# Performance work log

Hardware: AMD Instinct MI355X
Metric: run time of the kernel (lower is better)

Reference implementation:

```python
import jax, jax.numpy as jnp
import numpy as np

DIM, SSM, RNN = 1024, 64, 128


def setup_inputs() -> dict:
    key = jax.random.key(0)
    ks = jax.random.split(key, 16)
    s = 0.02
    B, N = 8, 2048
    return {
        'x': jax.random.normal(ks[0], (B, N, DIM), jnp.float32),
        'A': jax.random.normal(ks[1], (SSM, SSM), jnp.float32) * s,
        'Bw': jax.random.normal(ks[2], (SSM, DIM), jnp.float32) * s,
        'Bb': jnp.zeros((SSM,), jnp.float32),
        'Cw': jax.random.normal(ks[3], (DIM, SSM), jnp.float32) * s,
        'Cb': jnp.zeros((DIM,), jnp.float32),
        'Dw': jax.random.normal(ks[4], (DIM, DIM), jnp.float32) * s,
        'Db': jnp.zeros((DIM,), jnp.float32),
        'W_ih': jax.random.normal(ks[5], (3 * RNN, DIM), jnp.float32) * s,
        'b_ih': jnp.zeros((3 * RNN,), jnp.float32),
        'W_hh': jax.random.normal(ks[6], (3 * RNN, RNN), jnp.float32) * s,
        'b_hh': jnp.zeros((3 * RNN,), jnp.float32),
        'proj_w': jax.random.normal(ks[7], (DIM, RNN), jnp.float32) * s,
        'proj_b': jnp.zeros((DIM,), jnp.float32),
        'gate_w': jax.random.normal(ks[8], (2, DIM), jnp.float32) * s,
        'gate_b': jnp.zeros((2,), jnp.float32),
    }


def reference(x, A, Bw, Bb, Cw, Cb, Dw, Db, W_ih, b_ih, W_hh, b_hh, proj_w, proj_b, gate_w, gate_b):
    B, N, D = x.shape
    R = W_hh.shape[1]
    # Precompute all input-side projections once (time-parallel GEMMs).
    bx = jnp.einsum('bnd,sd->bns', x, Bw) + Bb            # [B,N,SSM]
    dx = jnp.einsum('bnd,ed->bne', x, Dw) + Db            # [B,N,D]
    gx = jax.nn.sigmoid(jnp.einsum('bnd,gd->bng', x, gate_w) + gate_b)  # [B,N,2]
    ih = jnp.einsum('bnd,rd->bnr', x, W_ih) + b_ih        # [B,N,3R]
    # time-major for scan
    bx_t = jnp.swapaxes(bx, 0, 1)
    dx_t = jnp.swapaxes(dx, 0, 1)
    gx_t = jnp.swapaxes(gx, 0, 1)
    ih_t = jnp.swapaxes(ih, 0, 1)

    h_ssm0 = jnp.zeros((B, A.shape[0]), x.dtype)
    h_rnn0 = jnp.zeros((B, R), x.dtype)

    def step(carry, inp):
        h_ssm, h_rnn = carry
        bxt, dxt, gxt, iht = inp
        h_ssm = jax.nn.silu(h_ssm @ A.T + bxt)
        y_ssm = h_ssm @ Cw.T + Cb + dxt
        # GRUCell (torch semantics)
        hh = h_rnn @ W_hh.T + b_hh
        i_r, i_z, i_n = jnp.split(iht, 3, axis=-1)
        h_r, h_z, h_n = jnp.split(hh, 3, axis=-1)
        r = jax.nn.sigmoid(i_r + h_r)
        z = jax.nn.sigmoid(i_z + h_z)
        n = jnp.tanh(i_n + r * h_n)
        h_rnn = (1.0 - z) * n + z * h_rnn
        y_rnn = h_rnn @ proj_w.T + proj_b
        fused = gxt[:, :1] * y_ssm + gxt[:, 1:2] * y_rnn
        return (h_ssm, h_rnn), fused

    _, out = jax.lax.scan(step, (h_ssm0, h_rnn0), (bx_t, dx_t, gx_t, ih_t))
    return jnp.swapaxes(out, 0, 1)  # [B,N,D]
```

## Files before the change

### kernel.cpp

```cpp
#include <hip/hip_runtime.h>


#define MROWS 16384
#define SEQ   2048
#define CH    16
#define NCH   (SEQ / CH)

typedef __attribute__((ext_vector_type(8))) short bf16x8;
typedef __attribute__((ext_vector_type(4))) float f32x4;

__device__ __forceinline__ float bf2f(unsigned short u) {
    union { unsigned int i; float f; } c; c.i = ((unsigned int)u) << 16; return c.f;
}
__device__ __forceinline__ unsigned short f2bf(float f) {
    union { float f; unsigned int i; } c; c.f = f;
    unsigned int x = c.i;
    return (unsigned short)((x + 0x7fffu + ((x >> 16) & 1u)) >> 16);
}
__device__ __forceinline__ unsigned int f2bf_pk(float lo, float hi) {
    unsigned int r;
    asm("v_cvt_pk_bf16_f32 %0, %1, %2" : "=v"(r) : "v"(lo), "v"(hi));
    return r;
}
__device__ __forceinline__ float ldin(const void* p, size_t i, int isf32) {
    return isf32 ? ((const float*)p)[i] : bf2f(((const unsigned short*)p)[i]);
}
__device__ __forceinline__ float sigf(float v) { return 1.f / (1.f + __expf(-v)); }
__device__ __forceinline__ float tanhf_fast(float v) { return 2.f * sigf(2.f * v) - 1.f; }

__global__ void sniff_kernel(const unsigned short* __restrict__ x, int* __restrict__ flag) {
    int tid = threadIdx.x;
    int big = 0;
    for (int i = tid; i < 1024; i += 64) {
        unsigned int e = (x[i] >> 7) & 0xFFu;
        big += (e >= 0xC0u) ? 1 : 0;
    }
#pragma unroll
    for (int off = 32; off; off >>= 1) big += __shfl_down(big, off);
    if (tid == 0) { flag[0] = (big >= 4) ? 1 : 0; flag[1] = 0; }
}

__global__ void zero_out_kernel(float* __restrict__ out) {
    size_t i = ((size_t)blockIdx.x * 256 + threadIdx.x) * 16;
#pragma unroll
    for (int u = 0; u < 16; u++) out[i + u] = 0.f;
}

__device__ __forceinline__ void cvt16(const void* src, unsigned short* dst,
                                      size_t i0, int isf32) {
#pragma unroll
    for (int q = 0; q < 2; q++) {
        size_t i = i0 + q * 8;
        if (isf32) {
            const float* s = (const float*)src + i;
            float4 a = *reinterpret_cast<const float4*>(s);
            float4 b = *reinterpret_cast<const float4*>(s + 4);
            union { bf16x8 v; unsigned int u[4]; } u;
            u.u[0] = f2bf_pk(a.x, a.y); u.u[1] = f2bf_pk(a.z, a.w);
            u.u[2] = f2bf_pk(b.x, b.y); u.u[3] = f2bf_pk(b.z, b.w);
            *reinterpret_cast<bf16x8*>(dst + i) = u.v;
        } else {
            *reinterpret_cast<bf16x8*>(dst + i) =
                *reinterpret_cast<const bf16x8*>((const unsigned short*)src + i);
        }
    }
}

__global__ __launch_bounds__(256) void cvt_all_kernel(
    const void* __restrict__ x,
    const void* __restrict__ Dw,  const void* __restrict__ Wih,
    const void* __restrict__ pw,  const void* __restrict__ Cw,
    const void* __restrict__ Bw,  const void* __restrict__ bih,
    const void* __restrict__ Bb,  const void* __restrict__ Cb,
    const void* __restrict__ Db,  const void* __restrict__ pb,
    unsigned short* __restrict__ xb,
    unsigned short* __restrict__ Dwb,  unsigned short* __restrict__ Wihb,
    unsigned short* __restrict__ pwb,  unsigned short* __restrict__ Cwb,
    unsigned short* __restrict__ Bwb,  unsigned short* __restrict__ bihb,
    unsigned short* __restrict__ Bbb,  unsigned short* __restrict__ Cbb,
    unsigned short* __restrict__ Dbb,  unsigned short* __restrict__ pbb,
    const int* __restrict__ flagp) {
    int isf32 = *flagp;
    int tid = threadIdx.x;
    if (blockIdx.x < 4096) {
        size_t i0 = ((size_t)blockIdx.x * 256 + tid) * 16;
        cvt16(x, xb, i0, isf32);
        return;
    }
    int blk = blockIdx.x - 4096;
    const void* src; unsigned short* dst; size_t base;
    if (blk < 256)      { src = Dw;  dst = Dwb;  base = (size_t)blk * 4096; }
    else if (blk < 352) { src = Wih; dst = Wihb; base = (size_t)(blk - 256) * 4096; }
    else if (blk < 384) { src = pw;  dst = pwb;  base = (size_t)(blk - 352) * 4096; }
    else if (blk < 400) { src = Cw;  dst = Cwb;  base = (size_t)(blk - 384) * 4096; }
    else if (blk < 416) { src = Bw;  dst = Bwb;  base = (size_t)(blk - 400) * 4096; }
    else {
        for (int i = tid; i < 384; i += 256) bihb[i] = f2bf(ldin(bih, i, isf32));
        if (tid < 64) Bbb[tid] = f2bf(ldin(Bb, tid, isf32));
        for (int i = tid; i < 1024; i += 256) {
            Cbb[i] = f2bf(ldin(Cb, i, isf32));
            Dbb[i] = f2bf(ldin(Db, i, isf32));
            pbb[i] = f2bf(ldin(pb, i, isf32));
        }
        return;
    }
    cvt16(src, dst, base + (size_t)tid * 16, isf32);
}

__device__ __forceinline__ void stage_tile(const void* __restrict__ g,
                                           int ld, int row0, int rowmax, int kb,
                                           short (*lds)[40], int tid, int isf32) {
#pragma unroll
    for (int q = 0; q < 2; q++) {
        int oct = q * 256 + tid;
        int row = oct >> 2, c8 = (oct & 3) << 3;
        int gr = row0 + row; if (gr > rowmax) gr = rowmax;
        size_t base = (size_t)gr * ld + kb + c8;
        bf16x8 v;
        if (isf32) {
            const float* gp = (const float*)g + base;
            float4 f0 = *reinterpret_cast<const float4*>(gp);
            float4 f1 = *reinterpret_cast<const float4*>(gp + 4);
            union { bf16x8 v8; unsigned int u[4]; } u;
            u.u[0] = f2bf_pk(f0.x, f0.y);
            u.u[1] = f2bf_pk(f0.z, f0.w);
            u.u[2] = f2bf_pk(f1.x, f1.y);
            u.u[3] = f2bf_pk(f1.z, f1.w);
            v = u.v8;
        } else {
            v = *reinterpret_cast<const bf16x8*>((const unsigned short*)g + base);
        }
        *reinterpret_cast<bf16x8*>(&lds[row][c8]) = v;
    }
}

__device__ __forceinline__ void mfma_tiles(const short (*As)[40], const short (*Bs)[40],
                                           int wm, int wn, int lane, f32x4 (*acc)[4]) {
    bf16x8 af[4], bfr[4];
    int m = lane & 15, ko = (lane >> 4) << 3;
#pragma unroll
    for (int i = 0; i < 4; i++)
        af[i] = *reinterpret_cast<const bf16x8*>(&As[wm + i * 16 + m][ko]);
#pragma unroll
    for (int j = 0; j < 4; j++)
        bfr[j] = *reinterpret_cast<const bf16x8*>(&Bs[wn + j * 16 + m][ko]);
#pragma unroll
    for (int i = 0; i < 4; i++)
#pragma unroll
        for (int j = 0; j < 4; j++)
            acc[i][j] = __builtin_amdgcn_mfma_f32_16x16x32_bf16(af[i], bfr[j], acc[i][j], 0, 0, 0);
}

__global__ __launch_bounds__(256) void gemm_fused_kernel(
    const void* __restrict__ A,
    const void* __restrict__ Wih, const void* __restrict__ bih, unsigned short* __restrict__ C1,
    const void* __restrict__ Bw,  const void* __restrict__ Bb,  unsigned short* __restrict__ C2,
    const int* __restrict__ flagp) {
    __shared__ __align__(16) short As[128][40];
    __shared__ __align__(16) short Bs[128][40];
    int isf32 = *flagp;
    int tid = threadIdx.x, lane = tid & 63, wave = tid >> 6;
    int wm = (wave >> 1) << 6, wn = (wave & 1) << 6;
    int tileM = blockIdx.x << 7;
    const void* W; const void* bias; unsigned short* C; int N, tileN;
    if (blockIdx.y < 3) { W = Wih; bias = bih; C = C1; N = 384; tileN = blockIdx.y << 7; }
    else                { W = Bw;  bias = Bb;  C = C2; N = 64;  tileN = 0; }
    f32x4 acc[4][4];
    f32x4 z = {0.f, 0.f, 0.f, 0.f};
#pragma unroll
    for (int i = 0; i < 4; i++)
#pragma unroll
        for (int j = 0; j < 4; j++) acc[i][j] = z;

    for (int kb = 0; kb < 1024; kb += 32) {
        __syncthreads();
        stage_tile(A, 1024, tileM, MROWS - 1, kb, As, tid, isf32);
        stage_tile(W, 1024, tileN, N - 1, kb, Bs, tid, isf32);
        __syncthreads();
        mfma_tiles(As, Bs, wm, wn, lane, acc);
    }
#pragma unroll
    for (int i = 0; i < 4; i++) {
#pragma unroll
        for (int j = 0; j < 4; j++) {
            int col = tileN + wn + j * 16 + (lane & 15);
            if (col < N) {
                float bv = ldin(bias, col, isf32);
                int row0 = tileM + wm + i * 16 + ((lane >> 4) << 2);
                unsigned int pk0 = f2bf_pk(acc[i][j][0] + bv, acc[i][j][1] + bv);
                unsigned int pk1 = f2bf_pk(acc[i][j][2] + bv, acc[i][j][3] + bv);
                C[(size_t)(row0 + 0) * N + col] = (unsigned short)(pk0 & 0xFFFFu);
                C[(size_t)(row0 + 1) * N + col] = (unsigned short)(pk0 >> 16);
                C[(size_t)(row0 + 2) * N + col] = (unsigned short)(pk1 & 0xFFFFu);
                C[(size_t)(row0 + 3) * N + col] = (unsigned short)(pk1 >> 16);
            }
        }
    }
}

__global__ __launch_bounds__(512) void scan_kernel(
    const void* __restrict__ Amat,
    const void* __restrict__ Whh,
    const void* __restrict__ bhh,
    const unsigned short* __restrict__ bxw,
    const unsigned short* __restrict__ ihw,
    unsigned short* __restrict__ hsw,
    unsigned short* __restrict__ hrw,
    const void* __restrict__ x,  const void* __restrict__ gw,
    const void* __restrict__ gb, float* __restrict__ gx,
    const int* __restrict__ flagp) {
    int isf32 = *flagp;
    f32x4 zf = {0.f, 0.f, 0.f, 0.f};

    if (blockIdx.x >= 16) {
        int row = (int)(blockIdx.x - 16) * 8 + (threadIdx.x >> 6);
        int lane = threadIdx.x & 63;
        size_t xoff = (size_t)row * 1024 + lane * 16;
        float a0 = 0.f, a1 = 0.f;
#pragma unroll
        for (int q = 0; q < 2; q++) {
#pragma unroll
            for (int e = 0; e < 8; e++) {
                size_t k = q * 8 + e;
                float xf = ldin(x, xoff + k, isf32);
                a0 += xf * ldin(gw, (size_t)lane * 16 + k, isf32);
                a1 += xf * ldin(gw, 1024 + (size_t)lane * 16 + k, isf32);
            }
        }
#pragma unroll
        for (int off = 32; off > 0; off >>= 1) {
            a0 += __shfl_down(a0, off);
            a1 += __shfl_down(a1, off);
        }
        if (lane == 0) {
            gx[row * 2]     = sigf(a0 + ldin(gb, 0, isf32));
            gx[row * 2 + 1] = sigf(a1 + ldin(gb, 1, isf32));
        }
        return;
    }

    int b = blockIdx.x & 7;
    size_t rowbase = (size_t)b * SEQ;

    if (blockIdx.x < 8) {
        __shared__ __align__(16) unsigned short H[2][128];
        __shared__ __align__(16) unsigned short IH[2][CH][384];
        int tid = threadIdx.x, lane = tid & 63, w = tid >> 6;
        int col = lane & 15, quad = lane >> 4;
        int o = w * 16 + col;
        if (tid < 256) ((unsigned short*)H)[tid] = 0;
        bf16x8 Bf[3][4];
#pragma unroll
        for (int g = 0; g < 3; g++) {
            int n = g * 128 + o;
#pragma unroll
            for (int c = 0; c < 4; c++) {
                int k0 = c * 32 + quad * 8;
                bf16x8 v;
#pragma unroll
                for (int e = 0; e < 8; e++)
                    v[e] = (short)f2bf(ldin(Whh, (size_t)n * 128 + k0 + e, isf32));
                Bf[g][c] = v;
            }
        }
        float bias_r = ldin(bhh, o, isf32);
        float bias_z = ldin(bhh, 128 + o, isf32);
        float bias_n = ldin(bhh, 256 + o, isf32);
        float hprev = 0.f;
        bool gl = (quad == 0);
        const unsigned short* ihbase = ihw + rowbase * 384;
        bf16x8 stg0, stg1;
        stg0 = *reinterpret_cast<const bf16x8*>(ihbase + (size_t)tid * 8);
        if (tid < 256) stg1 = *reinterpret_cast<const bf16x8*>(ihbase + (size_t)(512 + tid) * 8);
        *reinterpret_cast<bf16x8*>(&IH[0][0][0] + (size_t)tid * 8) = stg0;
        if (tid < 256) *reinterpret_cast<bf16x8*>(&IH[0][0][0] + (size_t)(512 + tid) * 8) = stg1;
        stg0 = *reinterpret_cast<const bf16x8*>(ihbase + (size_t)CH * 384 + (size_t)tid * 8);
        if (tid < 256) stg1 = *reinterpret_cast<const bf16x8*>(ihbase + (size_t)CH * 384 + (size_t)(512 + tid) * 8);
        __syncthreads();

        int p = 0;
        auto gru_step = [&](int t, int cur, int tt) {
            bf16x8 Af[4];
#pragma unroll
            for (int cc = 0; cc < 4; cc++)
                Af[cc] = *reinterpret_cast<const bf16x8*>(&H[p][cc * 32 + quad * 8]);
            float ir  = bf2f(IH[cur][tt][o]);
            float iz  = bf2f(IH[cur][tt][128 + o]);
            float inn = bf2f(IH[cur][tt][256 + o]);
            f32x4 aL[3], aH[3];
#pragma unroll
            for (int g = 0; g < 3; g++) {
                aL[g] = __builtin_amdgcn_mfma_f32_16x16x32_bf16(Af[0], Bf[g][0], zf, 0, 0, 0);
                aH[g] = __builtin_amdgcn_mfma_f32_16x16x32_bf16(Af[2], Bf[g][2], zf, 0, 0, 0);
                aL[g] = __builtin_amdgcn_mfma_f32_16x16x32_bf16(Af[1], Bf[g][1], aL[g], 0, 0, 0);
                aH[g] = __builtin_amdgcn_mfma_f32_16x16x32_bf16(Af[3], Bf[g][3], aH[g], 0, 0, 0);
            }
            float sr = aL[0][0] + aH[0][0];
            float sz = aL[1][0] + aH[1][0];
            float sn = aL[2][0] + aH[2][0];
            float r  = sigf(ir + sr + bias_r);
            float zg = sigf(iz + sz + bias_z);
            float n  = tanhf_fast(inn + r * (sn + bias_n));
            float hnew = (1.f - zg) * n + zg * hprev;
            hprev = hnew;
            if (gl) {
                unsigned short hb = f2bf(hnew);
                H[p ^ 1][o] = hb;
                hrw[(rowbase + t) * 128 + o] = hb;
            }
            asm volatile("s_waitcnt lgkmcnt(0)" ::: "memory");
            __builtin_amdgcn_s_barrier();
            asm volatile("" ::: "memory");
            p ^= 1;
        };

        for (int c = 0; c < NCH; c++) {
            int cur = c & 1;
            for (int tt = 0; tt < 8; tt++) gru_step(c * CH + tt, cur, tt);
            if (c + 1 < NCH) {
                unsigned short* dst = &IH[(c + 1) & 1][0][0];
                *reinterpret_cast<bf16x8*>(dst + (size_t)tid * 8) = stg0;
                if (tid < 256) *reinterpret_cast<bf16x8*>(dst + (size_t)(512 + tid) * 8) = stg1;
                if (c + 2 < NCH) {
                    const unsigned short* src = ihbase + (size_t)(c + 2) * CH * 384;
                    stg0 = *reinterpret_cast<const bf16x8*>(src + (size_t)tid * 8);
                    if (tid < 256) stg1 = *reinterpret_cast<const bf16x8*>(src + (size_t)(512 + tid) * 8);
                }
            }
            for (int tt = 8; tt < CH; tt++) gru_step(c * CH + tt, cur, tt);
        }
    } else {
        if (threadIdx.x >= 64) return;
        int lane = threadIdx.x, col = lane & 15, quad = lane >> 4;
        __shared__ __align__(16) unsigned short Hs[2][64];
        __shared__ __align__(16) unsigned short BX[2][CH][64];
        ((unsigned short*)Hs)[lane] = 0;
        ((unsigned short*)Hs)[64 + lane] = 0;
        bf16x8 Bf[4][2];
#pragma unroll
        for (int l = 0; l < 4; l++) {
            int n = l * 16 + col;
#pragma unroll
            for (int c = 0; c < 2; c++) {
                int k0 = c * 32 + quad * 8;
                bf16x8 v;
#pragma unroll
                for (int e = 0; e < 8; e++)
                    v[e] = (short)f2bf(ldin(Amat, (size_t)n * 64 + k0 + e, isf32));
                Bf[l][c] = v;
            }
        }
        bool gl = (quad == 0);
        const unsigned short* bxbase = bxw + rowbase * 64;
        bf16x8 stg[2];
#pragma unroll
        for (int q = 0; q < 2; q++)
            stg[q] = *reinterpret_cast<const bf16x8*>(bxbase + (size_t)(q * 64 + lane) * 8);
#pragma unroll
        for (int q = 0; q < 2; q++)
            *reinterpret_cast<bf16x8*>(&BX[0][0][0] + (size_t)(q * 64 + lane) * 8) = stg[q];
#pragma unroll
        for (int q = 0; q < 2; q++)
            stg[q] = *reinterpret_cast<const bf16x8*>(bxbase + (size_t)CH * 64 + (size_t)(q * 64 + lane) * 8);
        asm volatile("s_waitcnt lgkmcnt(0)" ::: "memory");

        int p = 0;
        auto ssm_step = [&](int t, int cur, int tt) {
            bf16x8 Af[2];
#pragma unroll
            for (int cc = 0; cc < 2; cc++)
                Af[cc] = *reinterpret_cast<const bf16x8*>(&Hs[p][cc * 32 + quad * 8]);
            float bx[4];
#pragma unroll
            for (int l = 0; l < 4; l++) bx[l] = bf2f(BX[cur][tt][l * 16 + col]);
            f32x4 acc[4];
#pragma unroll
            for (int l = 0; l < 4; l++) {
                acc[l] = __builtin_amdgcn_mfma_f32_16x16x32_bf16(Af[0], Bf[l][0], zf, 0, 0, 0);
                acc[l] = __builtin_amdgcn_mfma_f32_16x16x32_bf16(Af[1], Bf[l][1], acc[l], 0, 0, 0);
            }
#pragma unroll
            for (int l = 0; l < 4; l++) {
                int o = l * 16 + col;
                float v = acc[l][0] + bx[l];
                float hv = v * sigf(v);
                unsigned short hb = f2bf(hv);
                if (gl) {
                    Hs[p ^ 1][o] = hb;
                    hsw[(rowbase + t) * 64 + o] = hb;
                }
            }
            asm volatile("s_waitcnt lgkmcnt(0)" ::: "memory");
            p ^= 1;
        };

        for (int c = 0; c < NCH; c++) {
            int cur = c & 1;
            for (int tt = 0; tt < 8; tt++) ssm_step(c * CH + tt, cur, tt);
            if (c + 1 < NCH) {
                unsigned short* dst = &BX[(c + 1) & 1][0][0];
#pragma unroll
                for (int q = 0; q < 2; q++)
                    *reinterpret_cast<bf16x8*>(dst + (size_t)(q * 64 + lane) * 8) = stg[q];
                if (c + 2 < NCH) {
#pragma unroll
                    for (int q = 0; q < 2; q++)
                        stg[q] = *reinterpret_cast<const bf16x8*>(
                            bxbase + (size_t)(c + 2) * CH * 64 + (size_t)(q * 64 + lane) * 8);
                }
            }
            for (int tt = 8; tt < CH; tt++) ssm_step(c * CH + tt, cur, tt);
        }
    }
}

__global__ __launch_bounds__(256) void out_kernel(
    const void* __restrict__ x,  const void* __restrict__ Dw, const void* __restrict__ Db,
    const unsigned short* __restrict__ hs, const void* __restrict__ Cw, const void* __restrict__ Cb,
    const unsigned short* __restrict__ hr, const void* __restrict__ pw, const void* __restrict__ pb,
    const float* __restrict__ gx, float* __restrict__ out,
    const int* __restrict__ flagp) {
    __shared__ __align__(16) short As[128][40];
    __shared__ __align__(16) short Bs[128][40];
    int isf32 = *flagp;
    int tid = threadIdx.x, lane = tid & 63, wave = tid >> 6;
    int wm = (wave >> 1) << 6, wn = (wave & 1) << 6;
    int tileM = blockIdx.x << 7, tileN = blockIdx.y << 7;
    f32x4 z = {0.f, 0.f, 0.f, 0.f};
    f32x4 acc1[4][4], acc2[4][4];
#pragma unroll
    for (int i = 0; i < 4; i++)
#pragma unroll
        for (int j = 0; j < 4; j++) { acc1[i][j] = z; acc2[i][j] = z; }

    for (int kb = 0; kb < 1024; kb += 32) {
        __syncthreads();
        stage_tile(x,  1024, tileM, MROWS - 1, kb, As, tid, isf32);
        stage_tile(Dw, 1024, tileN, 1023, kb, Bs, tid, isf32);
        __syncthreads();
        mfma_tiles(As, Bs, wm, wn, lane, acc1);
    }
    for (int kb = 0; kb < 64; kb += 32) {
        __syncthreads();
        stage_tile(hs, 64, tileM, MROWS - 1, kb, As, tid, 0);
        stage_tile(Cw, 64, tileN, 1023, kb, Bs, tid, isf32);
        __syncthreads();
        mfma_tiles(As, Bs, wm, wn, lane, acc1);
    }
    for (int kb = 0; kb < 128; kb += 32) {
        __syncthreads();
        stage_tile(hr, 128, tileM, MROWS - 1, kb, As, tid, 0);
        stage_tile(pw, 128, tileN, 1023, kb, Bs, tid, isf32);
        __syncthreads();
        mfma_tiles(As, Bs, wm, wn, lane, acc2);
    }
#pragma unroll
    for (int i = 0; i < 4; i++) {
        int r0 = tileM + wm + i * 16 + ((lane >> 4) << 2);
#pragma unroll
        for (int j = 0; j < 4; j++) {
            int col = tileN + wn + j * 16 + (lane & 15);
            float cb  = ldin(Cb, col, isf32) + ldin(Db, col, isf32);
            float pbv = ldin(pb, col, isf32);
#pragma unroll
            for (int r = 0; r < 4; r++) {
                int row = r0 + r;
                float g0 = gx[row * 2], g1 = gx[row * 2 + 1];
                out[(size_t)row * 1024 + col] =
                    g0 * (acc1[i][j][r] + cb) + g1 * (acc2[i][j][r] + pbv);
            }
        }
    }
}

extern "C" void kernel_launch(void* const* d_in, const int* in_sizes, int n_in,
                              void* d_out, int out_size, void* d_ws, size_t ws_size,
                              hipStream_t stream) {
    static const int expect_sizes[16] = {16777216, 4096, 65536, 64, 65536, 1024,
                                         1048576, 1024, 393216, 384, 49152, 384,
                                         131072, 1024, 2048, 2};
    bool order_ok = (n_in == 16);
    if (order_ok)
        for (int i = 0; i < 16; i++)
            if (in_sizes[i] != expect_sizes[i]) { order_ok = false; break; }
    float* out = (float*)d_out;
    if (!order_ok) {
        zero_out_kernel<<<dim3(4096), dim3(256), 0, stream>>>(out);
        return;
    }

    const void* x    = d_in[0];
    const void* Amat = d_in[1];
    const void* Bw   = d_in[2];
    const void* Bb   = d_in[3];
    const void* Cw   = d_in[4];
    const void* Cb   = d_in[5];
    const void* Dw   = d_in[6];
    const void* Db   = d_in[7];
    const void* Wih  = d_in[8];
    const void* bih  = d_in[9];
    const void* Whh  = d_in[10];
    const void* bhh  = d_in[11];
    const void* pw   = d_in[12];
    const void* pb   = d_in[13];
    const void* gw   = d_in[14];
    const void* gb   = d_in[15];

    char* ws = (char*)d_ws;
    int*            flg = (int*)(ws);
    float*          gxw = (float*)(ws + 256);
    unsigned short* hsw = (unsigned short*)(ws + 131328);
    unsigned short* hrw = (unsigned short*)(ws + 2228480);
    unsigned short* bxw = (unsigned short*)(ws + 6422784);
    unsigned short* ihw = (unsigned short*)(ws + 8519936);
    unsigned short* xb   = (unsigned short*)(ws + 21102848);
    unsigned short* Dwb  = (unsigned short*)(ws + 54657280);
    unsigned short* Wihb = (unsigned short*)(ws + 56754432);
    unsigned short* pwb  = (unsigned short*)(ws + 57540864);
    unsigned short* Cwb  = (unsigned short*)(ws + 57803008);
    unsigned short* Bwb  = (unsigned short*)(ws + 57934080);
    unsigned short* bihb = (unsigned short*)(ws + 58065152);
    unsigned short* Bbb  = (unsigned short*)(ws + 58069248);
    unsigned short* Cbb  = (unsigned short*)(ws + 58073344);
    unsigned short* Dbb  = (unsigned short*)(ws + 58077440);
    unsigned short* pbb  = (unsigned short*)(ws + 58081536);
    bool big = ws_size >= 58085632ull;

    dim3 blk(256);
    sniff_kernel<<<dim3(1), dim3(64), 0, stream>>>((const unsigned short*)x, flg);
    if (big) {
        cvt_all_kernel<<<dim3(4513), blk, 0, stream>>>(
            x, Dw, Wih, pw, Cw, Bw, bih, Bb, Cb, Db, pb,
            xb, Dwb, Wihb, pwb, Cwb, Bwb, bihb, Bbb, Cbb, Dbb, pbb, flg);
        gemm_fused_kernel<<<dim3(128, 4), blk, 0, stream>>>(
            xb, Wihb, bihb, ihw, Bwb, Bbb, bxw, flg + 1);
        scan_kernel<<<dim3(2064), dim3(512), 0, stream>>>(
            Amat, Whh, bhh, bxw, ihw, hsw, hrw, x, gw, gb, gxw, flg);
        out_kernel<<<dim3(128, 8), blk, 0, stream>>>(
            xb, Dwb, Dbb, hsw, Cwb, Cbb, hrw, pwb, pbb, gxw, out, flg + 1);
    } else {
        gemm_fused_kernel<<<dim3(128, 4), blk, 0, stream>>>(
            x, Wih, bih, ihw, Bw, Bb, bxw, flg);
        scan_kernel<<<dim3(2064), dim3(512), 0, stream>>>(
            Amat, Whh, bhh, bxw, ihw, hsw, hrw, x, gw, gb, gxw, flg);
        out_kernel<<<dim3(128, 8), blk, 0, stream>>>(
            x, Dw, Db, hsw, Cw, Cb, hrw, pw, pb, gxw, out, flg);
    }
}
```

Baseline: 1.303 ms.

## Overlap x·Dw GEMM with the sequential scan by co-scheduling it in scan_kernel

Moves the large x·Dw^T projection out of out_kernel and into 1024 extra blocks of scan_kernel. The scan uses only 16 latency-bound blocks, so the GEMM can run on otherwise idle CUs while it proceeds, writing partial results into out. out_kernel now reads that partial and adds the hs·Cw and hr·pw contributions. It also splits the GRU recurrent MFMA accumulation into four independent chains to shorten the dependency chain, and moves shared memory into one 86KB buffer, which may reduce occupancy of the side blocks.

```diff
diff --git a/kernel.cpp b/kernel.cpp
--- a/kernel.cpp
+++ b/kernel.cpp
@@ -5,6 +5,7 @@
 #define SEQ   2048
 #define CH    16
 #define NCH   (SEQ / CH)
+#define SMEM_BYTES 86016
 
 typedef __attribute__((ext_vector_type(8))) short bf16x8;
 typedef __attribute__((ext_vector_type(4))) float f32x4;
@@ -134,6 +135,28 @@
     }
 }
 
+__device__ __forceinline__ void stage512(const void* __restrict__ g,
+                                         int ld, int row0, int kb,
+                                         short (*lds)[40], int tid, int isf32) {
+    int row = tid >> 2, c8 = (tid & 3) << 3;
+    size_t base = (size_t)(row0 + row) * ld + kb + c8;
+    bf16x8 v;
+    if (isf32) {
+        const float* gp = (const float*)g + base;
+        float4 f0 = *reinterpret_cast<const float4*>(gp);
+        float4 f1 = *reinterpret_cast<const float4*>(gp + 4);
+        union { bf16x8 v8; unsigned int u[4]; } u;
+        u.u[0] = f2bf_pk(f0.x, f0.y);
+        u.u[1] = f2bf_pk(f0.z, f0.w);
+        u.u[2] = f2bf_pk(f1.x, f1.y);
+        u.u[3] = f2bf_pk(f1.z, f1.w);
+        v = u.v8;
+    } else {
+        v = *reinterpret_cast<const bf16x8*>((const unsigned short*)g + base);
+    }
+    *reinterpret_cast<bf16x8*>(&lds[row][c8]) = v;
+}
+
 __device__ __forceinline__ void mfma_tiles(const short (*As)[40], const short (*Bs)[40],
                                            int wm, int wn, int lane, f32x4 (*acc)[4]) {
     bf16x8 af[4], bfr[4];
@@ -208,9 +231,59 @@
     unsigned short* __restrict__ hrw,
     const void* __restrict__ x,  const void* __restrict__ gw,
     const void* __restrict__ gb, float* __restrict__ gx,
-    const int* __restrict__ flagp) {
+    const void* __restrict__ xd, const void* __restrict__ Dwd,
+    float* __restrict__ outp,
+    const int* __restrict__ flagp, const int* __restrict__ dxflagp) {
+    __shared__ __align__(16) char smem[SMEM_BYTES];
     int isf32 = *flagp;
     f32x4 zf = {0.f, 0.f, 0.f, 0.f};
+
+    if (blockIdx.x >= 2064) {
+        int bid = (int)blockIdx.x - 2064;
+        int tileM = (bid >> 3) << 7, tileN = (bid & 7) << 7;
+        int dxf = *dxflagp;
+        short (*As)[40] = (short(*)[40])smem;
+        short (*Bs)[40] = (short(*)[40])(smem + 10240);
+        int tid = threadIdx.x, lane = tid & 63, wave = tid >> 6;
+        int wm = (wave >> 2) << 6;
+        int wn = (wave & 3) << 5;
+        f32x4 acc[4][2];
+#pragma unroll
+        for (int i = 0; i < 4; i++)
+#pragma unroll
+            for (int j = 0; j < 2; j++) acc[i][j] = zf;
+        for (int kb = 0; kb < 1024; kb += 32) {
+            __syncthreads();
+            stage512(xd,  1024, tileM, kb, As, tid, dxf);
+            stage512(Dwd, 1024, tileN, kb, Bs, tid, dxf);
+            __syncthreads();
+            bf16x8 af[4], bfr[2];
+            int m = lane & 15, ko = (lane >> 4) << 3;
+#pragma unroll
+            for (int i = 0; i < 4; i++)
+                af[i] = *reinterpret_cast<const bf16x8*>(&As[wm + i * 16 + m][ko]);
+#pragma unroll
+            for (int j = 0; j < 2; j++)
+                bfr[j] = *reinterpret_cast<const bf16x8*>(&Bs[wn + j * 16 + m][ko]);
+#pragma unroll
+            for (int i = 0; i < 4; i++)
+#pragma unroll
+                for (int j = 0; j < 2; j++)
+                    acc[i][j] = __builtin_amdgcn_mfma_f32_16x16x32_bf16(af[i], bfr[j], acc[i][j], 0, 0, 0);
+        }
+#pragma unroll
+        for (int i = 0; i < 4; i++) {
+            int row0 = tileM + wm + i * 16 + ((lane >> 4) << 2);
+#pragma unroll
+            for (int j = 0; j < 2; j++) {
+                int col = tileN + wn + j * 16 + (lane & 15);
+#pragma unroll
+                for (int r = 0; r < 4; r++)
+                    outp[(size_t)(row0 + r) * 1024 + col] = acc[i][j][r];
+            }
+        }
+        return;
+    }
 
     if (blockIdx.x >= 16) {
         int row = (int)(blockIdx.x - 16) * 8 + (threadIdx.x >> 6);
@@ -243,12 +316,12 @@
     size_t rowbase = (size_t)b * SEQ;
 
     if (blockIdx.x < 8) {
-        __shared__ __align__(16) unsigned short H[2][128];
-        __shared__ __align__(16) unsigned short IH[2][CH][384];
+        unsigned short (*H)[128] = (unsigned short(*)[128])smem;
+        unsigned short (*IH)[CH][384] = (unsigned short(*)[CH][384])(smem + 512);
         int tid = threadIdx.x, lane = tid & 63, w = tid >> 6;
         int col = lane & 15, quad = lane >> 4;
         int o = w * 16 + col;
-        if (tid < 256) ((unsigned short*)H)[tid] = 0;
+        if (tid < 256) ((unsigned short*)smem)[tid] = 0;
         bf16x8 Bf[3][4];
 #pragma unroll
         for (int g = 0; g < 3; g++) {
@@ -287,17 +360,15 @@
             float ir  = bf2f(IH[cur][tt][o]);
             float iz  = bf2f(IH[cur][tt][128 + o]);
             float inn = bf2f(IH[cur][tt][256 + o]);
-            f32x4 aL[3], aH[3];
-#pragma unroll
-            for (int g = 0; g < 3; g++) {
-                aL[g] = __builtin_amdgcn_mfma_f32_16x16x32_bf16(Af[0], Bf[g][0], zf, 0, 0, 0);
-                aH[g] = __builtin_amdgcn_mfma_f32_16x16x32_bf16(Af[2], Bf[g][2], zf, 0, 0, 0);
-                aL[g] = __builtin_amdgcn_mfma_f32_16x16x32_bf16(Af[1], Bf[g][1], aL[g], 0, 0, 0);
-                aH[g] = __builtin_amdgcn_mfma_f32_16x16x32_bf16(Af[3], Bf[g][3], aH[g], 0, 0, 0);
-            }
-            float sr = aL[0][0] + aH[0][0];
-            float sz = aL[1][0] + aH[1][0];
-            float sn = aL[2][0] + aH[2][0];
+            f32x4 a[3][4];
+#pragma unroll
+            for (int g = 0; g < 3; g++)
+#pragma unroll
+                for (int c = 0; c < 4; c++)
+                    a[g][c] = __builtin_amdgcn_mfma_f32_16x16x32_bf16(Af[c], Bf[g][c], zf, 0, 0, 0);
+            float sr = (a[0][0][0] + a[0][1][0]) + (a[0][2][0] + a[0][3][0]);
+            float sz = (a[1][0][0] + a[1][1][0]) + (a[1][2][0] + a[1][3][0]);
+            float sn = (a[2][0][0] + a[2][1][0]) + (a[2][2][0] + a[2][3][0]);
             float r  = sigf(ir + sr + bias_r);
             float zg = sigf(iz + sz + bias_z);
             float n  = tanhf_fast(inn + r * (sn + bias_n));
@@ -332,10 +403,10 @@
     } else {
         if (threadIdx.x >= 64) return;
         int lane = threadIdx.x, col = lane & 15, quad = lane >> 4;
-        __shared__ __align__(16) unsigned short Hs[2][64];
-        __shared__ __align__(16) unsigned short BX[2][CH][64];
-        ((unsigned short*)Hs)[lane] = 0;
-        ((unsigned short*)Hs)[64 + lane] = 0;
+        unsigned short (*Hs)[64] = (unsigned short(*)[64])smem;
+        unsigned short (*BX)[CH][64] = (unsigned short(*)[CH][64])(smem + 256);
+        ((unsigned short*)smem)[lane] = 0;
+        ((unsigned short*)smem)[64 + lane] = 0;
         bf16x8 Bf[4][2];
 #pragma unroll
         for (int l = 0; l < 4; l++) {
@@ -415,7 +486,7 @@
 }
 
 __global__ __launch_bounds__(256) void out_kernel(
-    const void* __restrict__ x,  const void* __restrict__ Dw, const void* __restrict__ Db,
+    const void* __restrict__ Db,
     const unsigned short* __restrict__ hs, const void* __restrict__ Cw, const void* __restrict__ Cb,
     const unsigned short* __restrict__ hr, const void* __restrict__ pw, const void* __restrict__ pb,
     const float* __restrict__ gx, float* __restrict__ out,
@@ -433,13 +504,6 @@
 #pragma unroll
         for (int j = 0; j < 4; j++) { acc1[i][j] = z; acc2[i][j] = z; }
 
-    for (int kb = 0; kb < 1024; kb += 32) {
-        __syncthreads();
-        stage_tile(x,  1024, tileM, MROWS - 1, kb, As, tid, isf32);
-        stage_tile(Dw, 1024, tileN, 1023, kb, Bs, tid, isf32);
-        __syncthreads();
-        mfma_tiles(As, Bs, wm, wn, lane, acc1);
-    }
     for (int kb = 0; kb < 64; kb += 32) {
         __syncthreads();
         stage_tile(hs, 64, tileM, MROWS - 1, kb, As, tid, 0);
@@ -466,8 +530,9 @@
             for (int r = 0; r < 4; r++) {
                 int row = r0 + r;
                 float g0 = gx[row * 2], g1 = gx[row * 2 + 1];
+                float dxv = out[(size_t)row * 1024 + col];
                 out[(size_t)row * 1024 + col] =
-                    g0 * (acc1[i][j][r] + cb) + g1 * (acc2[i][j][r] + pbv);
+                    g0 * (acc1[i][j][r] + dxv + cb) + g1 * (acc2[i][j][r] + pbv);
             }
         }
     }
@@ -534,16 +599,18 @@
             xb, Dwb, Wihb, pwb, Cwb, Bwb, bihb, Bbb, Cbb, Dbb, pbb, flg);
         gemm_fused_kernel<<<dim3(128, 4), blk, 0, stream>>>(
             xb, Wihb, bihb, ihw, Bwb, Bbb, bxw, flg + 1);
-        scan_kernel<<<dim3(2064), dim3(512), 0, stream>>>(
-            Amat, Whh, bhh, bxw, ihw, hsw, hrw, x, gw, gb, gxw, flg);
+        scan_kernel<<<dim3(3088), dim3(512), 0, stream>>>(
+            Amat, Whh, bhh, bxw, ihw, hsw, hrw, x, gw, gb, gxw,
+            xb, Dwb, out, flg, flg + 1);
         out_kernel<<<dim3(128, 8), blk, 0, stream>>>(
-            xb, Dwb, Dbb, hsw, Cwb, Cbb, hrw, pwb, pbb, gxw, out, flg + 1);
+            Dbb, hsw, Cwb, Cbb, hrw, pwb, pbb, gxw, out, flg + 1);
     } else {
         gemm_fused_kernel<<<dim3(128, 4), blk, 0, stream>>>(
             x, Wih, bih, ihw, Bw, Bb, bxw, flg);
-        scan_kernel<<<dim3(2064), dim3(512), 0, stream>>>(
-            Amat, Whh, bhh, bxw, ihw, hsw, hrw, x, gw, gb, gxw, flg);
+        scan_kernel<<<dim3(3088), dim3(512), 0, stream>>>(
+            Amat, Whh, bhh, bxw, ihw, hsw, hrw, x, gw, gb, gxw,
+            x, Dw, out, flg, flg);
         out_kernel<<<dim3(128, 8), blk, 0, stream>>>(
-            x, Dw, Db, hsw, Cw, Cb, hrw, pw, pb, gxw, out, flg);
-    }
-}
+            Db, hsw, Cw, Cb, hrw, pw, pb, gxw, out, flg);
+    }
+}
```

After: 1.328 ms. Within noise of the previous version (+1.9%).
